# Kernel tuning notes

Hardware: AMD Instinct MI355X
Metric: run time of the kernel (lower is better)

The kernel has to match this reference:

```python
import jax, jax.numpy as jnp
import numpy as np

PI = 3.141592653589793
DIM = 512          # entity/relation dim
HID = 2048         # MLP hidden dim
NREL = 500         # number of relations
NBASE = 30         # number of relation bases
B = 1024           # batch
EMB_RANGE = 0.0275 # (gamma+eps)/dim, ConE convention
AXIS_SCALE = 1.0
ARG_SCALE = 1.0
LN_EPS = 1e-5


def _ln(x):
    # LayerNorm, elementwise_affine=False
    m = x.mean(-1, keepdims=True)
    v = ((x - m) ** 2).mean(-1, keepdims=True)
    return (x - m) / jnp.sqrt(v + LN_EPS)


def _to_axis(x):
    return jnp.tanh(x) * PI


def _to_arg(x):
    return jnp.tanh(2 * x) * (PI / 2) + PI / 2


def _angle_scale(x, scale):
    return x / EMB_RANGE * scale


def setup_inputs() -> dict:
    key = jax.random.key(0)
    ks = jax.random.split(key, 16)
    D2 = 2 * DIM
    inp = {
        "source_embedding_axis": jax.random.normal(ks[0], (B, DIM), jnp.float32),
        "source_embedding_arg": jax.random.normal(ks[1], (B, DIM), jnp.float32),
        "rel_indices": jax.random.randint(ks[2], (B,), 0, NREL, jnp.int64)
        if jax.config.jax_enable_x64
        else jax.random.randint(ks[2], (B,), 0, NREL, jnp.int32),
        # rtrans branch params
        "rel_base": jax.random.normal(ks[3], (NBASE, D2, D2), jnp.float32) / np.sqrt(D2),
        "rel_att": jax.random.normal(ks[4], (NREL, NBASE), jnp.float32) * 0.05,
        "rel_bias": jax.random.normal(ks[5], (NBASE, D2), jnp.float32) * 0.05,
        # mlp branch params
        "rel_axis_embedding": jax.random.uniform(ks[6], (NREL, DIM), jnp.float32, -EMB_RANGE, EMB_RANGE),
        "rel_arg_embedding": jax.random.uniform(ks[7], (NREL, DIM), jnp.float32, -EMB_RANGE, EMB_RANGE),
        "W1": jax.random.normal(ks[8], (HID, D2), jnp.float32) * 0.02,
        "b1": jnp.zeros((HID,), jnp.float32),
        "W2": jax.random.normal(ks[9], (HID, HID), jnp.float32) * 0.02,
        "b2": jnp.zeros((HID,), jnp.float32),
        "W0": jax.random.normal(ks[10], (D2, HID), jnp.float32) * 0.02,
        "b0": jnp.zeros((D2,), jnp.float32),
        # attention fusion params
        "Wa1": jax.random.normal(ks[11], (DIM, D2), jnp.float32) * 0.02,
        "ba1": jnp.zeros((DIM,), jnp.float32),
        "Wa2": jax.random.normal(ks[12], (D2, DIM), jnp.float32) * 0.02,
        "ba2": jnp.zeros((D2,), jnp.float32),
    }
    return inp


def reference(source_embedding_axis, source_embedding_arg, rel_indices,
              rel_base, rel_att, rel_bias,
              rel_axis_embedding, rel_arg_embedding,
              W1, b1, W2, b2, W0, b0, Wa1, ba1, Wa2, ba2):
    # ---- rtrans branch ----
    att = rel_att[rel_indices]                          # (B, NBASE)
    att = _to_axis(_angle_scale(att, ARG_SCALE))        # tanh * pi
    e = jnp.concatenate([source_embedding_axis, source_embedding_arg], axis=-1)  # (B, 2D)
    # original: project_r = einsum('br,rio->bio'); out = einsum('bio,bi->bo')
    # reassociated (same math, avoids (B,2D,2D) intermediate):
    tmp = jnp.einsum('bi,rio->bro', e, rel_base)        # (B, NBASE, 2D)
    out = jnp.einsum('br,bro->bo', att, tmp)            # (B, 2D)
    bias = jnp.einsum('br,ri->bi', att, rel_bias)
    x_rtrans = _ln(out + bias)                          # (B, 2D)

    # ---- mlp branch ----
    r_axis = _to_axis(_angle_scale(rel_axis_embedding[rel_indices], AXIS_SCALE))
    r_arg = _to_arg(_angle_scale(rel_arg_embedding[rel_indices], ARG_SCALE))
    h = jnp.concatenate([source_embedding_axis + r_axis,
                         source_embedding_arg + r_arg], axis=-1)   # (B, 2D)
    h = jax.nn.relu(h @ W1.T + b1)
    h = jax.nn.relu(h @ W2.T + b2)
    x_mlp = _ln(h @ W0.T + b0)                          # (B, 2D)

    # ---- attention fusion (att_mode == 'stack') ----
    x_att = jnp.stack([x_rtrans, x_mlp])                # (2, B, 2D)
    a = jax.nn.relu(x_att @ Wa1.T + ba1)                # (2, B, D)
    attention = jax.nn.softmax(a @ Wa2.T + ba2, axis=0) # softmax over the 2 branches
    x_merged = jnp.sum(attention * x_att, axis=0)       # (B, 2D)

    axis, arg = jnp.split(x_merged, 2, axis=-1)
    return _to_axis(axis), _to_arg(arg)
```

## Files before the change

kernel.cpp:

```cpp
#include <hip/hip_runtime.h>
#include <hip/hip_bf16.h>
#include <stdint.h>

#define PI_F 3.14159265358979f
#define EMBR 0.0275f
#define BATCH 1024
#define DIM 512
#define D2 1024
#define HID 2048
#define NB 30
#define K1 (NB * D2)
#define NZ 8

using short8 = __attribute__((ext_vector_type(8))) short;
using f32x4  = __attribute__((ext_vector_type(4))) float;

#define WAITVM(N) __builtin_amdgcn_s_waitcnt(((N) & 0xF) | (((N) >> 4) << 14) | (0x7 << 4) | (0xF << 8))

__device__ __forceinline__ ushort f2bf(float f) {
  uint32_t u = __builtin_bit_cast(uint32_t, f);
  u += 0x7fffu + ((u >> 16) & 1u);
  return (ushort)(u >> 16);
}

__device__ __forceinline__ void gld_lds16(const void* g, void* l) {
  __builtin_amdgcn_global_load_lds(
      (const __attribute__((address_space(1))) uint32_t*)(uintptr_t)g,
      (__attribute__((address_space(3))) uint32_t*)(uintptr_t)l, 16, 0, 0);
}

#define TR_BLKS 7680
#define PREP_BLKS 1024
#define W1F4 (HID * D2 / 4)
#define W2F4 (HID * HID / 4)
#define W0F4 (D2 * HID / 4)
#define WA1F4 (DIM * D2 / 4)
#define WA2F4 (D2 * DIM / 4)
#define CVT_BLKS ((W1F4 + W2F4 + W0F4 + WA1F4 + WA2F4) / 256)

__global__ __launch_bounds__(256) void mega_prep(
    const float* __restrict__ rel_base, ushort* __restrict__ RBt,
    const float* __restrict__ axis, const float* __restrict__ argp,
    const int* __restrict__ rel, const float* __restrict__ rel_att,
    const float* __restrict__ rel_ax, const float* __restrict__ rel_ar,
    float* __restrict__ attb, ushort* __restrict__ Ebf, ushort* __restrict__ h0,
    const float* __restrict__ W1, const float* __restrict__ W2,
    const float* __restrict__ W0, const float* __restrict__ Wa1,
    const float* __restrict__ Wa2,
    ushort* __restrict__ W1b, ushort* __restrict__ W2b, ushort* __restrict__ W0b,
    ushort* __restrict__ Wa1b, ushort* __restrict__ Wa2b) {
  __shared__ ushort ts[64][68];
  const int bid = blockIdx.x, t = threadIdx.x;
  if (bid < TR_BLKS) {
    const int c0 = (bid & 15) * 64, r0 = (bid >> 4) * 64;
    const int tc = (t & 15) * 4;
    const int tr = t >> 4;
#pragma unroll
    for (int j = 0; j < 4; ++j) {
      const int r = tr + j * 16;
      float4 v = *(const float4*)&rel_base[(size_t)(r0 + r) * D2 + c0 + tc];
      ushort4 o;
      o.x = f2bf(v.x); o.y = f2bf(v.y); o.z = f2bf(v.z); o.w = f2bf(v.w);
      *(ushort4*)&ts[r][tc] = o;
    }
    __syncthreads();
#pragma unroll
    for (int j = 0; j < 4; ++j) {
      const int c = tr + j * 16;
      ushort4 v;
      v.x = ts[tc + 0][c]; v.y = ts[tc + 1][c];
      v.z = ts[tc + 2][c]; v.w = ts[tc + 3][c];
      *(ushort4*)&RBt[(size_t)(c0 + c) * K1 + r0 + tc] = v;
    }
  } else if (bid < TR_BLKS + PREP_BLKS) {
    const int b = bid - TR_BLKS;
    const int ri = rel[b];
    if (t < NB)
      attb[b * 32 + t] = tanhf(rel_att[ri * NB + t] * (1.f / EMBR)) * PI_F;
    for (int i = t; i < DIM; i += 256) {
      const float ax = axis[(size_t)b * DIM + i];
      const float ag = argp[(size_t)b * DIM + i];
      Ebf[(size_t)b * D2 + i]       = f2bf(ax);
      Ebf[(size_t)b * D2 + DIM + i] = f2bf(ag);
      const float ra = rel_ax[(size_t)ri * DIM + i];
      const float rg = rel_ar[(size_t)ri * DIM + i];
      h0[(size_t)b * D2 + i] = f2bf(ax + tanhf(ra * (1.f / EMBR)) * PI_F);
      h0[(size_t)b * D2 + DIM + i] =
          f2bf(ag + tanhf(2.f * rg * (1.f / EMBR)) * (PI_F * 0.5f) + PI_F * 0.5f);
    }
  } else {
    int i = (bid - TR_BLKS - PREP_BLKS) * 256 + t;
    const float* s; ushort* d;
    if (i < W1F4) { s = W1; d = W1b; }
    else if ((i -= W1F4) < W2F4) { s = W2; d = W2b; }
    else if ((i -= W2F4) < W0F4) { s = W0; d = W0b; }
    else if ((i -= W0F4) < WA1F4) { s = Wa1; d = Wa1b; }
    else { i -= WA1F4; s = Wa2; d = Wa2b; }
    float4 v = ((const float4*)s)[i];
    ushort4 o;
    o.x = f2bf(v.x); o.y = f2bf(v.y); o.z = f2bf(v.z); o.w = f2bf(v.w);
    ((ushort4*)d)[i] = o;
  }
}

template <int EPI>
__global__ __launch_bounds__(256, 2) void gemm_nt(
    const ushort* __restrict__ A, const ushort* __restrict__ Bt,
    const float* __restrict__ bias, float* __restrict__ Cf,
    ushort* __restrict__ Cb, int M, int N, int K) {
  __shared__ ushort As[4][128 * 32];
  __shared__ ushort Bs[4][128 * 32];
  const int tid  = threadIdx.x;
  const int lane = tid & 63, wave = tid >> 6;
  const int wm = wave >> 1, wn = wave & 1;
  const int lrow = lane & 15, quad = lane >> 4;
  const int m0 = blockIdx.y * 128, n0 = blockIdx.x * 128;
  const int T = K >> 5;

  const int rr = lane >> 2;
  const int eo = (lane & 3) * 8;
  const int c1 = wave, c2 = wave + 4;
  const ushort* Ag1 = A  + (size_t)(m0 + c1 * 16 + rr) * K + eo;
  const ushort* Ag2 = A  + (size_t)(m0 + c2 * 16 + rr) * K + eo;
  const ushort* Bg1 = Bt + (size_t)(n0 + c1 * 16 + rr) * K + eo;
  const ushort* Bg2 = Bt + (size_t)(n0 + c2 * 16 + rr) * K + eo;

  auto issue = [&](int slot) {
    const int t  = (slot < T - 1) ? slot : T - 1;
    const int bf = slot & 3;
    const int kk = t << 5;
    gld_lds16(Ag1 + kk, &As[bf][c1 * 512]);
    gld_lds16(Ag2 + kk, &As[bf][c2 * 512]);
    gld_lds16(Bg1 + kk, &Bs[bf][c1 * 512]);
    gld_lds16(Bg2 + kk, &Bs[bf][c2 * 512]);
  };

  f32x4 acc[4][4] = {};
  issue(0); issue(1); issue(2);

  for (int t = 0; t < T; ++t) {
    WAITVM(8);
    __builtin_amdgcn_s_barrier();
    issue(t + 3);
    const ushort* as = As[t & 3];
    const ushort* bs = Bs[t & 3];
    short8 af[4], bq[4];
#pragma unroll
    for (int i = 0; i < 4; ++i) {
      af[i] = *(const short8*)&as[(wm * 64 + i * 16 + lrow) * 32 + quad * 8];
      bq[i] = *(const short8*)&bs[(wn * 64 + i * 16 + lrow) * 32 + quad * 8];
    }
#pragma unroll
    for (int mi = 0; mi < 4; ++mi)
#pragma unroll
      for (int ni = 0; ni < 4; ++ni)
        acc[mi][ni] = __builtin_amdgcn_mfma_f32_16x16x32_bf16(
            af[mi], bq[ni], acc[mi][ni], 0, 0, 0);
  }
  WAITVM(0);

  const int colBase = n0 + wn * 64;
  const int rowBase = m0 + wm * 64;
#pragma unroll
  for (int mi = 0; mi < 4; ++mi) {
#pragma unroll
    for (int ni = 0; ni < 4; ++ni) {
      const int col  = colBase + ni * 16 + lrow;
      const int row0 = rowBase + mi * 16 + quad * 4;
      const float bv = bias[col];
      if (EPI == 1) {
#pragma unroll
        for (int g = 0; g < 4; ++g)
          Cb[(size_t)(row0 + g) * N + col] = f2bf(fmaxf(acc[mi][ni][g] + bv, 0.f));
      } else {
#pragma unroll
        for (int g = 0; g < 4; ++g)
          Cf[(size_t)(row0 + g) * N + col] = acc[mi][ni][g] + bv;
      }
    }
  }
}

__global__ __launch_bounds__(256, 2) void gemm_rtrans(
    const ushort* __restrict__ E, const ushort* __restrict__ RBt,
    const float* __restrict__ attb, float* __restrict__ C1p) {
  __shared__ ushort As[4][128 * 32];
  __shared__ ushort Bs[4][128 * 32];
  __shared__ float attS[4 * 128];
  const int tid  = threadIdx.x;
  const int lane = tid & 63, wave = tid >> 6;
  const int wm = wave >> 1, wn = wave & 1;
  const int lrow = lane & 15, quad = lane >> 4;
  const int m0 = blockIdx.y * 128, n0 = blockIdx.x * 128;
  const int z = blockIdx.z;
  const int r_start = (z < 7) ? z * 4 : 27;
  const int r_cnt   = (z < 6) ? 4 : 3;
  const int T = r_cnt << 5;

  for (int idx = tid; idx < r_cnt * 128; idx += 256)
    attS[idx] = attb[(size_t)(m0 + (idx & 127)) * 32 + r_start + (idx >> 7)];

  const int rr = lane >> 2;
  const int eo = (lane & 3) * 8;
  const int c1 = wave, c2 = wave + 4;
  const ushort* Ag1 = E + (size_t)(m0 + c1 * 16 + rr) * D2 + eo;
  const ushort* Ag2 = E + (size_t)(m0 + c2 * 16 + rr) * D2 + eo;
  const ushort* Bg1 = RBt + (size_t)(n0 + c1 * 16 + rr) * K1 + eo;
  const ushort* Bg2 = RBt + (size_t)(n0 + c2 * 16 + rr) * K1 + eo;

  auto issue = [&](int slot) {
    const int t  = (slot < T - 1) ? slot : T - 1;
    const int bf = slot & 3;
    const int ka = (t & 31) << 5;
    const size_t kb = ((size_t)(r_start + (t >> 5)) << 10) + ka;
    gld_lds16(Ag1 + ka, &As[bf][c1 * 512]);
    gld_lds16(Ag2 + ka, &As[bf][c2 * 512]);
    gld_lds16(Bg1 + kb, &Bs[bf][c1 * 512]);
    gld_lds16(Bg2 + kb, &Bs[bf][c2 * 512]);
  };

  f32x4 acc[4][4] = {};
  f32x4 acc2[4][4] = {};
  issue(0); issue(1); issue(2);
  __syncthreads();

  for (int t = 0; t < T; ++t) {
    WAITVM(8);
    __builtin_amdgcn_s_barrier();
    issue(t + 3);
    const ushort* as = As[t & 3];
    const ushort* bs = Bs[t & 3];
    short8 af[4], bq[4];
#pragma unroll
    for (int i = 0; i < 4; ++i) {
      af[i] = *(const short8*)&as[(wm * 64 + i * 16 + lrow) * 32 + quad * 8];
      bq[i] = *(const short8*)&bs[(wn * 64 + i * 16 + lrow) * 32 + quad * 8];
    }
#pragma unroll
    for (int mi = 0; mi < 4; ++mi)
#pragma unroll
      for (int ni = 0; ni < 4; ++ni)
        acc[mi][ni] = __builtin_amdgcn_mfma_f32_16x16x32_bf16(
            af[mi], bq[ni], acc[mi][ni], 0, 0, 0);
    if ((t & 31) == 31) {
      const int rl = t >> 5;
#pragma unroll
      for (int mi = 0; mi < 4; ++mi)
#pragma unroll
        for (int g = 0; g < 4; ++g) {
          const float s = attS[rl * 128 + wm * 64 + mi * 16 + quad * 4 + g];
#pragma unroll
          for (int ni = 0; ni < 4; ++ni) {
            acc2[mi][ni][g] += s * acc[mi][ni][g];
            acc[mi][ni][g] = 0.f;
          }
        }
    }
  }
  WAITVM(0);

  float* dst = C1p + (size_t)z * BATCH * D2;
  const int colBase = n0 + wn * 64;
  const int rowBase = m0 + wm * 64;
#pragma unroll
  for (int mi = 0; mi < 4; ++mi)
#pragma unroll
    for (int ni = 0; ni < 4; ++ni) {
      const int col  = colBase + ni * 16 + lrow;
      const int row0 = rowBase + mi * 16 + quad * 4;
#pragma unroll
      for (int g = 0; g < 4; ++g)
        dst[(size_t)(row0 + g) * D2 + col] = acc2[mi][ni][g];
    }
}

__global__ __launch_bounds__(256) void reduce_ln_rt(
    const float* __restrict__ C1p, const float* __restrict__ att,
    const float* __restrict__ rel_bias, float* __restrict__ xf,
    ushort* __restrict__ Xb) {
  const int b = blockIdx.x, t = threadIdx.x;
  __shared__ float attS[NB];
  __shared__ float sa[4], sb[4];
  if (t < NB) attS[t] = att[b * 32 + t];
  __syncthreads();
  float v[4], sum = 0.f, sq = 0.f;
#pragma unroll
  for (int j = 0; j < 4; ++j) {
    const int o = j * 256 + t;
    float acc = 0.f;
#pragma unroll
    for (int s = 0; s < NZ; ++s)
      acc += C1p[((size_t)s * BATCH + b) * D2 + o];
    float bias = 0.f;
    for (int r = 0; r < NB; ++r) bias += attS[r] * rel_bias[r * D2 + o];
    acc += bias;
    v[j] = acc; sum += acc; sq += acc * acc;
  }
  const int lane = t & 63, wv = t >> 6;
  for (int off = 32; off > 0; off >>= 1) {
    sum += __shfl_down(sum, off, 64);
    sq  += __shfl_down(sq, off, 64);
  }
  if (lane == 0) { sa[wv] = sum; sb[wv] = sq; }
  __syncthreads();
  const float S = sa[0] + sa[1] + sa[2] + sa[3];
  const float Q = sb[0] + sb[1] + sb[2] + sb[3];
  const float mean = S / D2;
  const float inv = rsqrtf(fmaxf(Q / D2 - mean * mean, 0.f) + 1e-5f);
#pragma unroll
  for (int j = 0; j < 4; ++j) {
    const int o = j * 256 + t;
    const float y = (v[j] - mean) * inv;
    xf[(size_t)b * D2 + o] = y;
    Xb[(size_t)b * D2 + o] = f2bf(y);
  }
}

__global__ __launch_bounds__(256) void ln_rows(
    const float* __restrict__ G, float* __restrict__ xf, ushort* __restrict__ Xb) {
  const int b = blockIdx.x, t = threadIdx.x;
  __shared__ float sa[4], sb[4];
  float v[4], sum = 0.f, sq = 0.f;
#pragma unroll
  for (int j = 0; j < 4; ++j) {
    const int o = j * 256 + t;
    v[j] = G[(size_t)b * D2 + o];
    sum += v[j]; sq += v[j] * v[j];
  }
  const int lane = t & 63, wv = t >> 6;
  for (int off = 32; off > 0; off >>= 1) {
    sum += __shfl_down(sum, off, 64);
    sq  += __shfl_down(sq, off, 64);
  }
  if (lane == 0) { sa[wv] = sum; sb[wv] = sq; }
  __syncthreads();
  const float S = sa[0] + sa[1] + sa[2] + sa[3];
  const float Q = sb[0] + sb[1] + sb[2] + sb[3];
  const float mean = S / D2;
  const float inv = rsqrtf(fmaxf(Q / D2 - mean * mean, 0.f) + 1e-5f);
#pragma unroll
  for (int j = 0; j < 4; ++j) {
    const int o = j * 256 + t;
    const float y = (v[j] - mean) * inv;
    xf[(size_t)b * D2 + o] = y;
    Xb[(size_t)b * D2 + o] = f2bf(y);
  }
}

__global__ __launch_bounds__(256) void fuse_out(
    const float* __restrict__ L, const float* __restrict__ xrt,
    const float* __restrict__ xml, float* __restrict__ out) {
  const int b = blockIdx.x, t = threadIdx.x;
#pragma unroll
  for (int j = 0; j < 4; ++j) {
    const int o = j * 256 + t;
    const float l0 = L[(size_t)b * D2 + o];
    const float l1 = L[(size_t)(BATCH + b) * D2 + o];
    const float w0 = 1.f / (1.f + expf(l1 - l0));
    const float m = w0 * xrt[(size_t)b * D2 + o] +
                    (1.f - w0) * xml[(size_t)b * D2 + o];
    if (o < DIM)
      out[(size_t)b * DIM + o] = tanhf(m) * PI_F;
    else
      out[(size_t)BATCH * DIM + (size_t)b * DIM + (o - DIM)] =
          tanhf(2.f * m) * (PI_F * 0.5f) + PI_F * 0.5f;
  }
}

extern "C" void kernel_launch(void* const* d_in, const int* in_sizes, int n_in,
                              void* d_out, int out_size, void* d_ws, size_t ws_size,
                              hipStream_t stream) {
  (void)in_sizes; (void)n_in; (void)out_size; (void)ws_size;
  const float* s_axis   = (const float*)d_in[0];
  const float* s_arg    = (const float*)d_in[1];
  const int*   rel      = (const int*)d_in[2];
  const float* rel_base = (const float*)d_in[3];
  const float* rel_att  = (const float*)d_in[4];
  const float* rel_bias = (const float*)d_in[5];
  const float* rel_ax_e = (const float*)d_in[6];
  const float* rel_ar_e = (const float*)d_in[7];
  const float* W1 = (const float*)d_in[8];
  const float* b1 = (const float*)d_in[9];
  const float* W2 = (const float*)d_in[10];
  const float* b2 = (const float*)d_in[11];
  const float* W0 = (const float*)d_in[12];
  const float* b0 = (const float*)d_in[13];
  const float* Wa1 = (const float*)d_in[14];
  const float* ba1 = (const float*)d_in[15];
  const float* Wa2 = (const float*)d_in[16];
  const float* ba2 = (const float*)d_in[17];

  char* ws = (char*)d_ws;
  size_t off = 0;
  ushort* RBt  = (ushort*)(ws + off); off += (size_t)K1 * D2 * 2;
  float*  C1p  = (float*)(ws + off);  off += (size_t)NZ * BATCH * D2 * 4;
  ushort* Ebf  = (ushort*)(ws + off); off += (size_t)BATCH * D2 * 2;
  ushort* W1b  = (ushort*)(ws + off); off += (size_t)HID * D2 * 2;
  ushort* W2b  = (ushort*)(ws + off); off += (size_t)HID * HID * 2;
  ushort* W0b  = (ushort*)(ws + off); off += (size_t)D2 * HID * 2;
  ushort* Wa1b = (ushort*)(ws + off); off += (size_t)DIM * D2 * 2;
  ushort* Wa2b = (ushort*)(ws + off); off += (size_t)D2 * DIM * 2;
  ushort* h0   = (ushort*)(ws + off); off += (size_t)BATCH * D2 * 2;
  ushort* Xb   = (ushort*)(ws + off); off += (size_t)2 * BATCH * D2 * 2;
  float*  xrt  = (float*)(ws + off);  off += (size_t)BATCH * D2 * 4;
  float*  xml  = (float*)(ws + off);  off += (size_t)BATCH * D2 * 4;
  float*  attb = (float*)(ws + off);  off += (size_t)BATCH * 32 * 4;
  char* ali = (char*)C1p;
  ushort* H1  = (ushort*)ali; ali += (size_t)BATCH * HID * 2;
  ushort* H2  = (ushort*)ali; ali += (size_t)BATCH * HID * 2;
  float*  G0  = (float*)ali;  ali += (size_t)BATCH * D2 * 4;
  ushort* Aat = (ushort*)ali; ali += (size_t)2 * BATCH * DIM * 2;
  float*  Lg  = (float*)ali;  ali += (size_t)2 * BATCH * D2 * 4;

  mega_prep<<<TR_BLKS + PREP_BLKS + CVT_BLKS, 256, 0, stream>>>(
      rel_base, RBt, s_axis, s_arg, rel, rel_att, rel_ax_e, rel_ar_e,
      attb, Ebf, h0, W1, W2, W0, Wa1, Wa2, W1b, W2b, W0b, Wa1b, Wa2b);
  gemm_rtrans<<<dim3(D2 / 128, BATCH / 128, NZ), 256, 0, stream>>>(
      Ebf, RBt, attb, C1p);
  reduce_ln_rt<<<BATCH, 256, 0, stream>>>(C1p, attb, rel_bias, xrt, Xb);
  gemm_nt<1><<<dim3(HID / 128, BATCH / 128), 256, 0, stream>>>(
      h0, W1b, b1, nullptr, H1, BATCH, HID, D2);
  gemm_nt<1><<<dim3(HID / 128, BATCH / 128), 256, 0, stream>>>(
      H1, W2b, b2, nullptr, H2, BATCH, HID, HID);
  gemm_nt<2><<<dim3(D2 / 128, BATCH / 128), 256, 0, stream>>>(
      H2, W0b, b0, G0, nullptr, BATCH, D2, HID);
  ln_rows<<<BATCH, 256, 0, stream>>>(G0, xml, Xb + (size_t)BATCH * D2);
  gemm_nt<1><<<dim3(DIM / 128, 2 * BATCH / 128), 256, 0, stream>>>(
      Xb, Wa1b, ba1, nullptr, Aat, 2 * BATCH, DIM, D2);
  gemm_nt<2><<<dim3(D2 / 128, 2 * BATCH / 128), 256, 0, stream>>>(
      Aat, Wa2b, ba2, Lg, nullptr, 2 * BATCH, D2, DIM);
  fuse_out<<<BATCH, 256, 0, stream>>>(Lg, xrt, xml, (float*)d_out);
}
```

Before: 432.0 us.

## Recast relation-basis GEMM as wide-N GEMM with atomic attention-weighted reduction

The rel_base transpose is re-laid out so each basis forms a 1024-column slab. The rtrans contraction becomes a single GEMM of the batch against all 30 bases (N = 30*1024) with 128x256 tiles and a 3-stage LDS pipeline. Each tile scales its outputs by the per-row attention weight and atomically adds them into one zeroed output buffer, replacing the 8-way split partial buffers and their summation. This removes the partial-sum writes and reads and adds parallelism, at the cost of heavy float atomic traffic (30 adds per output element), a memset, and nondeterministic summation order.

```diff
diff --git a/kernel.cpp b/kernel.cpp
--- a/kernel.cpp
+++ b/kernel.cpp
@@ -10,7 +10,6 @@
 #define HID 2048
 #define NB 30
 #define K1 (NB * D2)
-#define NZ 8
 
 using short8 = __attribute__((ext_vector_type(8))) short;
 using f32x4  = __attribute__((ext_vector_type(4))) float;
@@ -70,7 +69,7 @@
       ushort4 v;
       v.x = ts[tc + 0][c]; v.y = ts[tc + 1][c];
       v.z = ts[tc + 2][c]; v.w = ts[tc + 3][c];
-      *(ushort4*)&RBt[(size_t)(c0 + c) * K1 + r0 + tc] = v;
+      *(ushort4*)&RBt[((size_t)((r0 & ~1023) + c0 + c)) * 1024 + (r0 & 1023) + tc] = v;
     }
   } else if (bid < TR_BLKS + PREP_BLKS) {
     const int b = bid - TR_BLKS;
@@ -181,101 +180,87 @@
   }
 }
 
-__global__ __launch_bounds__(256, 2) void gemm_rtrans(
-    const ushort* __restrict__ E, const ushort* __restrict__ RBt,
-    const float* __restrict__ attb, float* __restrict__ C1p) {
-  __shared__ ushort As[4][128 * 32];
-  __shared__ ushort Bs[4][128 * 32];
-  __shared__ float attS[4 * 128];
+__global__ __launch_bounds__(256, 2) void gemm_rt2(
+    const ushort* __restrict__ A,
+    const ushort* __restrict__ Bt,
+    const float* __restrict__ attb,
+    float* __restrict__ outrt) {
+  __shared__ ushort As[3][128 * 32];
+  __shared__ ushort Bs[3][256 * 32];
   const int tid  = threadIdx.x;
   const int lane = tid & 63, wave = tid >> 6;
   const int wm = wave >> 1, wn = wave & 1;
   const int lrow = lane & 15, quad = lane >> 4;
-  const int m0 = blockIdx.y * 128, n0 = blockIdx.x * 128;
-  const int z = blockIdx.z;
-  const int r_start = (z < 7) ? z * 4 : 27;
-  const int r_cnt   = (z < 6) ? 4 : 3;
-  const int T = r_cnt << 5;
-
-  for (int idx = tid; idx < r_cnt * 128; idx += 256)
-    attS[idx] = attb[(size_t)(m0 + (idx & 127)) * 32 + r_start + (idx >> 7)];
+  const int n0 = blockIdx.x * 256, m0 = blockIdx.y * 128;
+  const int r  = n0 >> 10;
+  const int K = 1024, T = 32;
 
   const int rr = lane >> 2;
   const int eo = (lane & 3) * 8;
-  const int c1 = wave, c2 = wave + 4;
-  const ushort* Ag1 = E + (size_t)(m0 + c1 * 16 + rr) * D2 + eo;
-  const ushort* Ag2 = E + (size_t)(m0 + c2 * 16 + rr) * D2 + eo;
-  const ushort* Bg1 = RBt + (size_t)(n0 + c1 * 16 + rr) * K1 + eo;
-  const ushort* Bg2 = RBt + (size_t)(n0 + c2 * 16 + rr) * K1 + eo;
+  const ushort* Ag0 = A  + (size_t)(m0 +   0 + wave * 16 + rr) * K + eo;
+  const ushort* Ag1 = A  + (size_t)(m0 +  64 + wave * 16 + rr) * K + eo;
+  const ushort* Bg0 = Bt + (size_t)(n0 +   0 + wave * 16 + rr) * K + eo;
+  const ushort* Bg1 = Bt + (size_t)(n0 +  64 + wave * 16 + rr) * K + eo;
+  const ushort* Bg2 = Bt + (size_t)(n0 + 128 + wave * 16 + rr) * K + eo;
+  const ushort* Bg3 = Bt + (size_t)(n0 + 192 + wave * 16 + rr) * K + eo;
 
   auto issue = [&](int slot) {
     const int t  = (slot < T - 1) ? slot : T - 1;
-    const int bf = slot & 3;
-    const int ka = (t & 31) << 5;
-    const size_t kb = ((size_t)(r_start + (t >> 5)) << 10) + ka;
-    gld_lds16(Ag1 + ka, &As[bf][c1 * 512]);
-    gld_lds16(Ag2 + ka, &As[bf][c2 * 512]);
-    gld_lds16(Bg1 + kb, &Bs[bf][c1 * 512]);
-    gld_lds16(Bg2 + kb, &Bs[bf][c2 * 512]);
+    const int bf = slot % 3;
+    const int kk = t << 5;
+    gld_lds16(Ag0 + kk, &As[bf][(  0 + wave * 16) * 32]);
+    gld_lds16(Ag1 + kk, &As[bf][( 64 + wave * 16) * 32]);
+    gld_lds16(Bg0 + kk, &Bs[bf][(  0 + wave * 16) * 32]);
+    gld_lds16(Bg1 + kk, &Bs[bf][( 64 + wave * 16) * 32]);
+    gld_lds16(Bg2 + kk, &Bs[bf][(128 + wave * 16) * 32]);
+    gld_lds16(Bg3 + kk, &Bs[bf][(192 + wave * 16) * 32]);
   };
 
-  f32x4 acc[4][4] = {};
-  f32x4 acc2[4][4] = {};
-  issue(0); issue(1); issue(2);
-  __syncthreads();
+  f32x4 acc[4][8] = {};
+  issue(0); issue(1);
 
   for (int t = 0; t < T; ++t) {
-    WAITVM(8);
+    WAITVM(6);
     __builtin_amdgcn_s_barrier();
-    issue(t + 3);
-    const ushort* as = As[t & 3];
-    const ushort* bs = Bs[t & 3];
-    short8 af[4], bq[4];
-#pragma unroll
-    for (int i = 0; i < 4; ++i) {
+    issue(t + 2);
+    const ushort* as = As[t % 3];
+    const ushort* bs = Bs[t % 3];
+    short8 af[4], bq[8];
+#pragma unroll
+    for (int i = 0; i < 4; ++i)
       af[i] = *(const short8*)&as[(wm * 64 + i * 16 + lrow) * 32 + quad * 8];
-      bq[i] = *(const short8*)&bs[(wn * 64 + i * 16 + lrow) * 32 + quad * 8];
-    }
+#pragma unroll
+    for (int i = 0; i < 8; ++i)
+      bq[i] = *(const short8*)&bs[(wn * 128 + i * 16 + lrow) * 32 + quad * 8];
 #pragma unroll
     for (int mi = 0; mi < 4; ++mi)
 #pragma unroll
-      for (int ni = 0; ni < 4; ++ni)
+      for (int ni = 0; ni < 8; ++ni)
         acc[mi][ni] = __builtin_amdgcn_mfma_f32_16x16x32_bf16(
             af[mi], bq[ni], acc[mi][ni], 0, 0, 0);
-    if ((t & 31) == 31) {
-      const int rl = t >> 5;
-#pragma unroll
-      for (int mi = 0; mi < 4; ++mi)
-#pragma unroll
-        for (int g = 0; g < 4; ++g) {
-          const float s = attS[rl * 128 + wm * 64 + mi * 16 + quad * 4 + g];
-#pragma unroll
-          for (int ni = 0; ni < 4; ++ni) {
-            acc2[mi][ni][g] += s * acc[mi][ni][g];
-            acc[mi][ni][g] = 0.f;
-          }
-        }
-    }
   }
   WAITVM(0);
 
-  float* dst = C1p + (size_t)z * BATCH * D2;
-  const int colBase = n0 + wn * 64;
+  const int colBase = n0 + wn * 128;
   const int rowBase = m0 + wm * 64;
 #pragma unroll
-  for (int mi = 0; mi < 4; ++mi)
-#pragma unroll
-    for (int ni = 0; ni < 4; ++ni) {
-      const int col  = colBase + ni * 16 + lrow;
+  for (int mi = 0; mi < 4; ++mi) {
+#pragma unroll
+    for (int ni = 0; ni < 8; ++ni) {
+      const int col = colBase + ni * 16 + lrow;
+      const int o   = col & 1023;
       const int row0 = rowBase + mi * 16 + quad * 4;
 #pragma unroll
-      for (int g = 0; g < 4; ++g)
-        dst[(size_t)(row0 + g) * D2 + col] = acc2[mi][ni][g];
-    }
+      for (int g = 0; g < 4; ++g) {
+        const float s = attb[(row0 + g) * 32 + r];
+        unsafeAtomicAdd(&outrt[(size_t)(row0 + g) * D2 + o], s * acc[mi][ni][g]);
+      }
+    }
+  }
 }
 
 __global__ __launch_bounds__(256) void reduce_ln_rt(
-    const float* __restrict__ C1p, const float* __restrict__ att,
+    const float* __restrict__ outrt, const float* __restrict__ att,
     const float* __restrict__ rel_bias, float* __restrict__ xf,
     ushort* __restrict__ Xb) {
   const int b = blockIdx.x, t = threadIdx.x;
@@ -287,10 +272,7 @@
 #pragma unroll
   for (int j = 0; j < 4; ++j) {
     const int o = j * 256 + t;
-    float acc = 0.f;
-#pragma unroll
-    for (int s = 0; s < NZ; ++s)
-      acc += C1p[((size_t)s * BATCH + b) * D2 + o];
+    float acc = outrt[(size_t)b * D2 + o];
     float bias = 0.f;
     for (int r = 0; r < NB; ++r) bias += attS[r] * rel_bias[r * D2 + o];
     acc += bias;
@@ -392,8 +374,8 @@
 
   char* ws = (char*)d_ws;
   size_t off = 0;
-  ushort* RBt  = (ushort*)(ws + off); off += (size_t)K1 * D2 * 2;
-  float*  C1p  = (float*)(ws + off);  off += (size_t)NZ * BATCH * D2 * 4;
+  ushort* RBt2 = (ushort*)(ws + off); off += (size_t)K1 * D2 * 2;
+  float*  outrt= (float*)(ws + off);  off += (size_t)BATCH * D2 * 4;
   ushort* Ebf  = (ushort*)(ws + off); off += (size_t)BATCH * D2 * 2;
   ushort* W1b  = (ushort*)(ws + off); off += (size_t)HID * D2 * 2;
   ushort* W2b  = (ushort*)(ws + off); off += (size_t)HID * HID * 2;
@@ -403,21 +385,22 @@
   ushort* h0   = (ushort*)(ws + off); off += (size_t)BATCH * D2 * 2;
   ushort* Xb   = (ushort*)(ws + off); off += (size_t)2 * BATCH * D2 * 2;
   float*  xrt  = (float*)(ws + off);  off += (size_t)BATCH * D2 * 4;
-  float*  xml  = (float*)(ws + off);  off += (size_t)BATCH * D2 * 4;
+  float*  xml  = (float*)(ws + off);  off += (size_t)BATCH * 32 * 4 + (size_t)BATCH * D2 * 4;
   float*  attb = (float*)(ws + off);  off += (size_t)BATCH * 32 * 4;
-  char* ali = (char*)C1p;
+  char* ali = (char*)RBt2;
   ushort* H1  = (ushort*)ali; ali += (size_t)BATCH * HID * 2;
   ushort* H2  = (ushort*)ali; ali += (size_t)BATCH * HID * 2;
   float*  G0  = (float*)ali;  ali += (size_t)BATCH * D2 * 4;
   ushort* Aat = (ushort*)ali; ali += (size_t)2 * BATCH * DIM * 2;
   float*  Lg  = (float*)ali;  ali += (size_t)2 * BATCH * D2 * 4;
 
+  hipMemsetAsync(outrt, 0, (size_t)BATCH * D2 * 4, stream);
   mega_prep<<<TR_BLKS + PREP_BLKS + CVT_BLKS, 256, 0, stream>>>(
-      rel_base, RBt, s_axis, s_arg, rel, rel_att, rel_ax_e, rel_ar_e,
+      rel_base, RBt2, s_axis, s_arg, rel, rel_att, rel_ax_e, rel_ar_e,
       attb, Ebf, h0, W1, W2, W0, Wa1, Wa2, W1b, W2b, W0b, Wa1b, Wa2b);
-  gemm_rtrans<<<dim3(D2 / 128, BATCH / 128, NZ), 256, 0, stream>>>(
-      Ebf, RBt, attb, C1p);
-  reduce_ln_rt<<<BATCH, 256, 0, stream>>>(C1p, attb, rel_bias, xrt, Xb);
+  gemm_rt2<<<dim3(K1 / 256, BATCH / 128), 256, 0, stream>>>(
+      Ebf, RBt2, attb, outrt);
+  reduce_ln_rt<<<BATCH, 256, 0, stream>>>(outrt, attb, rel_bias, xrt, Xb);
   gemm_nt<1><<<dim3(HID / 128, BATCH / 128), 256, 0, stream>>>(
       h0, W1b, b1, nullptr, H1, BATCH, HID, D2);
   gemm_nt<1><<<dim3(HID / 128, BATCH / 128), 256, 0, stream>>>(
```

Measured after the change: 488.5 us. 1.13x slower.

## Split rtrans GEMM over K slices, keep A fragments in registers across bases

Applied to the files above, without the earlier changes.

The relation-basis GEMM now assigns each z-block a 128-wide slice of the input dimension and loops over all 30 bases, instead of giving each z-block a group of bases over the full K. The A (entity) tile is loaded once into LDS and then into registers, and is reused for every basis, so only the B (rel_base) tiles are streamed through a 3-deep pipeline. Sched barriers are added to pin the load/MFMA ordering. The per-basis attention weights are all preloaded into LDS, which raises LDS use and may reduce occupancy.

```diff
diff --git a/kernel.cpp b/kernel.cpp
--- a/kernel.cpp
+++ b/kernel.cpp
@@ -16,6 +16,7 @@
 using f32x4  = __attribute__((ext_vector_type(4))) float;
 
 #define WAITVM(N) __builtin_amdgcn_s_waitcnt(((N) & 0xF) | (((N) >> 4) << 14) | (0x7 << 4) | (0xF << 8))
+#define SCHED_FENCE() __builtin_amdgcn_sched_barrier(0)
 
 __device__ __forceinline__ ushort f2bf(float f) {
   uint32_t u = __builtin_bit_cast(uint32_t, f);
@@ -181,81 +182,88 @@
   }
 }
 
-__global__ __launch_bounds__(256, 2) void gemm_rtrans(
-    const ushort* __restrict__ E, const ushort* __restrict__ RBt,
-    const float* __restrict__ attb, float* __restrict__ C1p) {
+__global__ __launch_bounds__(256, 2) void gemm_rt6(
+    const ushort* __restrict__ E,
+    const ushort* __restrict__ RBt,
+    const float* __restrict__ attb,
+    float* __restrict__ C1p) {
+  __shared__ ushort Bs[3][128 * 32];
   __shared__ ushort As[4][128 * 32];
-  __shared__ ushort Bs[4][128 * 32];
-  __shared__ float attS[4 * 128];
+  __shared__ float attL[NB * 128];
   const int tid  = threadIdx.x;
   const int lane = tid & 63, wave = tid >> 6;
   const int wm = wave >> 1, wn = wave & 1;
   const int lrow = lane & 15, quad = lane >> 4;
-  const int m0 = blockIdx.y * 128, n0 = blockIdx.x * 128;
-  const int z = blockIdx.z;
-  const int r_start = (z < 7) ? z * 4 : 27;
-  const int r_cnt   = (z < 6) ? 4 : 3;
-  const int T = r_cnt << 5;
-
-  for (int idx = tid; idx < r_cnt * 128; idx += 256)
-    attS[idx] = attb[(size_t)(m0 + (idx & 127)) * 32 + r_start + (idx >> 7)];
+  const int n0 = blockIdx.x * 128, m0 = blockIdx.y * 128, z = blockIdx.z;
 
   const int rr = lane >> 2;
   const int eo = (lane & 3) * 8;
-  const int c1 = wave, c2 = wave + 4;
-  const ushort* Ag1 = E + (size_t)(m0 + c1 * 16 + rr) * D2 + eo;
-  const ushort* Ag2 = E + (size_t)(m0 + c2 * 16 + rr) * D2 + eo;
-  const ushort* Bg1 = RBt + (size_t)(n0 + c1 * 16 + rr) * K1 + eo;
-  const ushort* Bg2 = RBt + (size_t)(n0 + c2 * 16 + rr) * K1 + eo;
-
+
+#pragma unroll
+  for (int j = 0; j < 2; ++j)
+#pragma unroll
+    for (int ks = 0; ks < 4; ++ks)
+      gld_lds16(E + (size_t)(m0 + j * 64 + wave * 16 + rr) * D2 + z * 128 + ks * 32 + eo,
+                &As[ks][(j * 64 + wave * 16) * 32]);
+
+  const ushort* Bg1 = RBt + (size_t)(n0 + wave * 16 + rr) * K1 + z * 128 + eo;
+  const ushort* Bg2 = Bg1 + (size_t)64 * K1;
   auto issue = [&](int slot) {
-    const int t  = (slot < T - 1) ? slot : T - 1;
-    const int bf = slot & 3;
-    const int ka = (t & 31) << 5;
-    const size_t kb = ((size_t)(r_start + (t >> 5)) << 10) + ka;
-    gld_lds16(Ag1 + ka, &As[bf][c1 * 512]);
-    gld_lds16(Ag2 + ka, &As[bf][c2 * 512]);
-    gld_lds16(Bg1 + kb, &Bs[bf][c1 * 512]);
-    gld_lds16(Bg2 + kb, &Bs[bf][c2 * 512]);
+    const int v  = (slot < 120) ? slot : 119;
+    const int bf = slot % 3;
+    const size_t ko = (size_t)(v >> 2) * 1024 + (v & 3) * 32;
+    gld_lds16(Bg1 + ko, &Bs[bf][(wave * 16) * 32]);
+    gld_lds16(Bg2 + ko, &Bs[bf][(64 + wave * 16) * 32]);
   };
-
-  f32x4 acc[4][4] = {};
+  issue(0); issue(1);
+
+  for (int idx = tid; idx < NB * 128; idx += 256)
+    attL[idx] = attb[(size_t)(m0 + (idx & 127)) * 32 + (idx >> 7)];
+
+  __syncthreads();
+
+  short8 af[4][4];
+#pragma unroll
+  for (int ks = 0; ks < 4; ++ks)
+#pragma unroll
+    for (int mi = 0; mi < 4; ++mi)
+      af[ks][mi] = *(const short8*)&As[ks][(wm * 64 + mi * 16 + lrow) * 32 + quad * 8];
+
+  f32x4 acc[4][4]  = {};
   f32x4 acc2[4][4] = {};
-  issue(0); issue(1); issue(2);
-  __syncthreads();
-
-  for (int t = 0; t < T; ++t) {
-    WAITVM(8);
-    __builtin_amdgcn_s_barrier();
-    issue(t + 3);
-    const ushort* as = As[t & 3];
-    const ushort* bs = Bs[t & 3];
-    short8 af[4], bq[4];
-#pragma unroll
-    for (int i = 0; i < 4; ++i) {
-      af[i] = *(const short8*)&as[(wm * 64 + i * 16 + lrow) * 32 + quad * 8];
-      bq[i] = *(const short8*)&bs[(wn * 64 + i * 16 + lrow) * 32 + quad * 8];
+
+  for (int r = 0; r < NB; ++r) {
+#pragma unroll
+    for (int ks = 0; ks < 4; ++ks) {
+      const int v = r * 4 + ks;
+      WAITVM(2);
+      __builtin_amdgcn_s_barrier();
+      SCHED_FENCE();
+      issue(v + 2);
+      const ushort* bs = Bs[v % 3];
+      short8 bq[4];
+#pragma unroll
+      for (int i = 0; i < 4; ++i)
+        bq[i] = *(const short8*)&bs[(wn * 64 + i * 16 + lrow) * 32 + quad * 8];
+#pragma unroll
+      for (int mi = 0; mi < 4; ++mi)
+#pragma unroll
+        for (int ni = 0; ni < 4; ++ni)
+          acc[mi][ni] = __builtin_amdgcn_mfma_f32_16x16x32_bf16(
+              af[ks][mi], bq[ni], acc[mi][ni], 0, 0, 0);
+      SCHED_FENCE();
     }
 #pragma unroll
     for (int mi = 0; mi < 4; ++mi)
 #pragma unroll
-      for (int ni = 0; ni < 4; ++ni)
-        acc[mi][ni] = __builtin_amdgcn_mfma_f32_16x16x32_bf16(
-            af[mi], bq[ni], acc[mi][ni], 0, 0, 0);
-    if ((t & 31) == 31) {
-      const int rl = t >> 5;
-#pragma unroll
-      for (int mi = 0; mi < 4; ++mi)
-#pragma unroll
-        for (int g = 0; g < 4; ++g) {
-          const float s = attS[rl * 128 + wm * 64 + mi * 16 + quad * 4 + g];
-#pragma unroll
-          for (int ni = 0; ni < 4; ++ni) {
-            acc2[mi][ni][g] += s * acc[mi][ni][g];
-            acc[mi][ni][g] = 0.f;
-          }
+      for (int g = 0; g < 4; ++g) {
+        const float s = attL[r * 128 + wm * 64 + mi * 16 + quad * 4 + g];
+#pragma unroll
+        for (int ni = 0; ni < 4; ++ni) {
+          acc2[mi][ni][g] += s * acc[mi][ni][g];
+          acc[mi][ni][g] = 0.f;
         }
-    }
+      }
   }
   WAITVM(0);
 
@@ -415,7 +423,7 @@
   mega_prep<<<TR_BLKS + PREP_BLKS + CVT_BLKS, 256, 0, stream>>>(
       rel_base, RBt, s_axis, s_arg, rel, rel_att, rel_ax_e, rel_ar_e,
       attb, Ebf, h0, W1, W2, W0, Wa1, Wa2, W1b, W2b, W0b, Wa1b, Wa2b);
-  gemm_rtrans<<<dim3(D2 / 128, BATCH / 128, NZ), 256, 0, stream>>>(
+  gemm_rt6<<<dim3(D2 / 128, BATCH / 128, NZ), 256, 0, stream>>>(
       Ebf, RBt, attb, C1p);
   reduce_ln_rt<<<BATCH, 256, 0, stream>>>(C1p, attb, rel_bias, xrt, Xb);
   gemm_nt<1><<<dim3(HID / 128, BATCH / 128), 256, 0, stream>>>(
```

After: 416.9 us. 3.5% less time.
